# Performance work log

Hardware: AMD Instinct MI355X
Metric: run time of the kernel (lower is better)

## Reference

```python
import jax, jax.numpy as jnp
import numpy as np

B, C, H, W, K = 8, 256, 128, 128, 9
P = K // 2
DN = ('NCHW', 'OIHW', 'NCHW')


def _dw(x, w, pad):
    # depthwise conv: w has shape (C,1,kh,kw), feature_group_count=C
    return jax.lax.conv_general_dilated(
        x, w, window_strides=(1, 1), padding=pad,
        dimension_numbers=DN, feature_group_count=C)


def setup_inputs() -> dict:
    key = jax.random.key(0)
    ks = jax.random.split(key, 6)
    s = 1.0 / np.sqrt(K)
    return {
        'x': jax.random.normal(ks[0], (B, C, H, W), dtype=jnp.float32),
        'wh1': jax.random.normal(ks[1], (C, 1, 1, K), dtype=jnp.float32) * s,
        'wh2': jax.random.normal(ks[2], (C, 1, 1, K), dtype=jnp.float32) * s,
        'wv1': jax.random.normal(ks[3], (C, 1, K, 1), dtype=jnp.float32) * s,
        'wv2': jax.random.normal(ks[4], (C, 1, K, 1), dtype=jnp.float32) * s,
        'wproj': jax.random.normal(ks[5], (C, 4 * C), dtype=jnp.float32) / np.sqrt(4 * C),
    }


def reference(x, wh1, wh2, wv1, wv2, wproj):
    pad_h = ((0, 0), (P, P))  # 1xK conv pads width
    pad_v = ((P, P), (0, 0))  # Kx1 conv pads height
    y = jnp.concatenate([
        _dw(x, wh1, pad_h),
        _dw(x, wh2, pad_h),
        _dw(x, wv1, pad_v),
        _dw(x, wv2, pad_v),
    ], axis=1)  # (B, 4C, H, W)
    out = jnp.einsum('oc,bchw->bohw', wproj, y)  # 1x1 projection
    return jax.nn.relu(out)
```

## Files before the change

### kernel.cpp

```cpp
#include <hip/hip_runtime.h>
#include <hip/hip_bf16.h>

#define BB 8
#define CC 256
#define HH 128
#define WW 128
#define KS 9
#define NPIX (BB*HH*WW)
#define KDIM (4*CC)

typedef __attribute__((ext_vector_type(8))) short bf16x8;
typedef __attribute__((ext_vector_type(4))) float f32x4;

static __device__ __forceinline__ unsigned short f2bf(float f) {
  union { float f; unsigned u; } v; v.f = f;
  unsigned r = v.u + 0x7FFF + ((v.u >> 16) & 1);
  return (unsigned short)(r >> 16);
}
static __device__ __forceinline__ float bf2f(unsigned short u) {
  union { unsigned u; float f; } v; v.u = ((unsigned)u) << 16;
  return v.f;
}

static __device__ __forceinline__ void gload_lds16(const void* g, void* l) {
  __builtin_amdgcn_global_load_lds(
      (const __attribute__((address_space(1))) void*)g,
      (__attribute__((address_space(3))) void*)l, 16, 0, 0);
}

__global__ void prep_kernel(const float* __restrict__ wproj,
                            unsigned short* __restrict__ Ap) {
  int idx = blockIdx.x * 256 + threadIdx.x;
  int o  = idx >> 10;
  int kp = idx & 1023;
  int c  = kp >> 2;
  int t  = kp & 3;
  Ap[idx] = f2bf(wproj[o * 1024 + t * 256 + c]);
}

__global__ void wprep_kernel(const float* __restrict__ wh1,
                             const float* __restrict__ wh2,
                             const float* __restrict__ wv1,
                             const float* __restrict__ wv2,
                             float* __restrict__ wt) {
  int idx = blockIdx.x * 256 + threadIdx.x;
  int c = idx & 255;
  int q = idx >> 8;
  int cv = q / 9, k = q % 9;
  const float* src = (cv == 0) ? wh1 : (cv == 1) ? wh2 : (cv == 2) ? wv1 : wv2;
  wt[idx] = src[c * KS + k];
}

__global__ __launch_bounds__(256)
void transpose_kernel(const float* __restrict__ x,
                      unsigned short* __restrict__ xt) {
  __shared__ float lds[64][65];
  int g   = blockIdx.x;
  int b   = g >> 10;
  int r   = g & 1023;
  int ct  = r >> 8;
  int hwt = r & 255;
  int c0  = ct * 64, hw0 = hwt * 64;
  const float* in = x + (size_t)b * CC * (HH * WW);
  unsigned short* outp = xt + (size_t)b * (HH * WW) * CC;

  int tr  = threadIdx.x >> 4;
  int tc4 = (threadIdx.x & 15) * 4;

#pragma unroll
  for (int s = 0; s < 4; ++s) {
    int row = tr + s * 16;
    float4 v = *(const float4*)(in + (size_t)(c0 + row) * (HH * WW) + hw0 + tc4);
    lds[row][tc4 + 0] = v.x; lds[row][tc4 + 1] = v.y;
    lds[row][tc4 + 2] = v.z; lds[row][tc4 + 3] = v.w;
  }
  __syncthreads();
#pragma unroll
  for (int s = 0; s < 4; ++s) {
    int row_o = tr + s * 16;
    ushort4 o;
    o.x = f2bf(lds[tc4 + 0][row_o]);
    o.y = f2bf(lds[tc4 + 1][row_o]);
    o.z = f2bf(lds[tc4 + 2][row_o]);
    o.w = f2bf(lds[tc4 + 3][row_o]);
    *(ushort4*)(outp + (size_t)(hw0 + row_o) * CC + c0 + tc4) = o;
  }
}

__global__ __launch_bounds__(256)
void conv_kernel(const unsigned short* __restrict__ xt,
                 const float* __restrict__ wt,
                 unsigned short* __restrict__ Y) {
  int g  = blockIdx.x;
  int sb = (g & 7) * 512 + (g >> 3);
  int w  = sb & 127;
  int tq = sb >> 7;
  int hs = tq & 3;
  int b  = tq >> 2;
  int c  = threadIdx.x;

  float W1[KS], W2[KS], W3[KS], W4[KS];
#pragma unroll
  for (int k = 0; k < KS; ++k) {
    W1[k] = wt[(0 * KS + k) * CC + c];
    W2[k] = wt[(1 * KS + k) * CC + c];
    W3[k] = wt[(2 * KS + k) * CC + c];
    W4[k] = wt[(3 * KS + k) * CC + c];
  }

  const unsigned short* xb = xt + (size_t)b * (HH * WW) * CC;
  int h0 = hs * 32;

  float vwin[9];
#pragma unroll
  for (int i = 0; i < 8; ++i) {
    int row = h0 - 4 + i;
    vwin[i] = (row >= 0) ? bf2f(xb[(size_t)(row * WW + w) * CC + c]) : 0.f;
  }

#pragma unroll
  for (int s = 0; s < 32; ++s) {
    int h  = h0 + s;
    int rv = h + 4;
    vwin[8] = (rv < HH) ? bf2f(xb[(size_t)(rv * WW + w) * CC + c]) : 0.f;

    float hwin[9];
#pragma unroll
    for (int j = 0; j < 9; ++j) {
      if (j == 4) { hwin[j] = vwin[4]; continue; }
      int wp = w - 4 + j;
      hwin[j] = (wp >= 0 && wp < WW) ? bf2f(xb[(size_t)(h * WW + wp) * CC + c]) : 0.f;
    }

    float s1 = 0.f, s2 = 0.f, s3 = 0.f, s4 = 0.f;
#pragma unroll
    for (int k = 0; k < KS; ++k) {
      s1 = fmaf(hwin[k], W1[k], s1);
      s2 = fmaf(hwin[k], W2[k], s2);
      s3 = fmaf(vwin[k], W3[k], s3);
      s4 = fmaf(vwin[k], W4[k], s4);
    }
    unsigned u0 = (unsigned)f2bf(s1) | ((unsigned)f2bf(s2) << 16);
    unsigned u1 = (unsigned)f2bf(s3) | ((unsigned)f2bf(s4) << 16);
    size_t p = (size_t)(b * (HH * WW) + h * WW + w);
    *(uint2*)(Y + p * KDIM + c * 4) = make_uint2(u0, u1);

#pragma unroll
    for (int i = 0; i < 8; ++i) vwin[i] = vwin[i + 1];
  }
}

__global__ __launch_bounds__(512)
void gemm_kernel(const unsigned short* __restrict__ Ap,
                 const unsigned short* __restrict__ Yg,
                 float* __restrict__ out) {
  __shared__ short As[256 * 64];
  __shared__ short Bs[128 * 64];

  int bid = blockIdx.x;
  int pt  = (bid & 7) * 128 + (bid >> 3);
  int tid  = threadIdx.x;
  int lane = tid & 63;
  int wv   = tid >> 6;
  int om   = wv & 3;
  int pn   = wv >> 2;
  int l15  = lane & 15;
  int kseg = lane >> 4;

  const short* A  = (const short*)Ap;
  const short* Bg = (const short*)Yg + (size_t)pt * 128 * KDIM;

  int srow = tid >> 3;
  int skc  = (tid & 7) * 8;

  f32x4 acc[4][4] = {};

  for (int k0 = 0; k0 < KDIM; k0 += 64) {
#pragma unroll
    for (int i = 0; i < 4; ++i) {
      int rr = i * 64 + srow;
      gload_lds16(A + (size_t)rr * KDIM + k0 + skc, &As[rr * 64 + skc]);
    }
#pragma unroll
    for (int i = 0; i < 2; ++i) {
      int rr = i * 64 + srow;
      gload_lds16(Bg + (size_t)rr * KDIM + k0 + skc, &Bs[rr * 64 + skc]);
    }
    __syncthreads();
#pragma unroll
    for (int kk = 0; kk < 2; ++kk) {
      bf16x8 af[4], bfr[4];
#pragma unroll
      for (int m = 0; m < 4; ++m)
        af[m] = *(const bf16x8*)&As[(om * 64 + m * 16 + l15) * 64 + kk * 32 + kseg * 8];
#pragma unroll
      for (int n = 0; n < 4; ++n)
        bfr[n] = *(const bf16x8*)&Bs[(pn * 64 + n * 16 + l15) * 64 + kk * 32 + kseg * 8];
#pragma unroll
      for (int m = 0; m < 4; ++m)
#pragma unroll
        for (int n = 0; n < 4; ++n)
          acc[m][n] = __builtin_amdgcn_mfma_f32_16x16x32_bf16(af[m], bfr[n],
                                                              acc[m][n], 0, 0, 0);
    }
    __syncthreads();
  }

  int b = pt >> 7, h = pt & 127;
#pragma unroll
  for (int m = 0; m < 4; ++m) {
#pragma unroll
    for (int n = 0; n < 4; ++n) {
#pragma unroll
      for (int r = 0; r < 4; ++r) {
        int o = om * 64 + m * 16 + kseg * 4 + r;
        int w = pn * 64 + n * 16 + l15;
        out[((size_t)(b * 256 + o) << 14) + (h << 7) + w] =
            fmaxf(acc[m][n][r], 0.f);
      }
    }
  }
}

extern "C" void kernel_launch(void* const* d_in, const int* in_sizes, int n_in,
                              void* d_out, int out_size, void* d_ws, size_t ws_size,
                              hipStream_t stream) {
  (void)in_sizes; (void)n_in; (void)out_size; (void)ws_size;
  const float* x     = (const float*)d_in[0];
  const float* wh1   = (const float*)d_in[1];
  const float* wh2   = (const float*)d_in[2];
  const float* wv1   = (const float*)d_in[3];
  const float* wv2   = (const float*)d_in[4];
  const float* wproj = (const float*)d_in[5];
  float* out = (float*)d_out;

  char* wsb = (char*)d_ws;
  unsigned short* Yg = (unsigned short*)wsb;
  unsigned short* Xt = (unsigned short*)(wsb + (size_t)NPIX * KDIM * 2);
  unsigned short* Ap = (unsigned short*)(wsb + (size_t)NPIX * KDIM * 2
                                             + (size_t)NPIX * CC * 2);
  float* Wt = (float*)(wsb + (size_t)NPIX * KDIM * 2
                           + (size_t)NPIX * CC * 2 + (size_t)CC * KDIM * 2);

  hipLaunchKernelGGL(prep_kernel, dim3(1024), dim3(256), 0, stream, wproj, Ap);
  hipLaunchKernelGGL(wprep_kernel, dim3(36), dim3(256), 0, stream,
                     wh1, wh2, wv1, wv2, Wt);
  hipLaunchKernelGGL(transpose_kernel, dim3(8192), dim3(256), 0, stream, x, Xt);
  hipLaunchKernelGGL(conv_kernel, dim3(4096), dim3(256), 0, stream, Xt, Wt, Yg);
  hipLaunchKernelGGL(gemm_kernel, dim3(1024), dim3(512), 0, stream, Ap, Yg, out);
}
```

Before: 605.6 us.

## Slide conv window along width and stage GEMM epilogue through LDS for vector stores

The conv kernel now gives each block one row and a 32-column strip, sliding the horizontal window along width and loading the vertical taps fresh for each pixel. Before, each block walked down 32 rows of one column. This changes the locality of the transposed input and makes consecutive Y writes contiguous per block. The GEMM epilogue now writes accumulators to LDS in 32-row chunks and reads them back so each thread issues two float4 stores per output row. This replaces the scattered scalar stores. The cost is eight extra LDS round trips with barriers, and more global loads per pixel in the conv, relying on the cache to absorb them.

```diff
diff --git a/kernel.cpp b/kernel.cpp
--- a/kernel.cpp
+++ b/kernel.cpp
@@ -91,13 +91,12 @@
 void conv_kernel(const unsigned short* __restrict__ xt,
                  const float* __restrict__ wt,
                  unsigned short* __restrict__ Y) {
-  int g  = blockIdx.x;
-  int sb = (g & 7) * 512 + (g >> 3);
-  int w  = sb & 127;
-  int tq = sb >> 7;
-  int hs = tq & 3;
-  int b  = tq >> 2;
-  int c  = threadIdx.x;
+  int g    = blockIdx.x;
+  int b    = g & 7;
+  int rest = g >> 3;
+  int h    = rest >> 2;
+  int ws   = rest & 3;
+  int c    = threadIdx.x;
 
   float W1[KS], W2[KS], W3[KS], W4[KS];
 #pragma unroll
@@ -109,27 +108,26 @@
   }
 
   const unsigned short* xb = xt + (size_t)b * (HH * WW) * CC;
-  int h0 = hs * 32;
-
-  float vwin[9];
-#pragma unroll
-  for (int i = 0; i < 8; ++i) {
-    int row = h0 - 4 + i;
-    vwin[i] = (row >= 0) ? bf2f(xb[(size_t)(row * WW + w) * CC + c]) : 0.f;
-  }
-
-#pragma unroll
+  int w0 = ws * 32;
+
+  float hwin[9];
+#pragma unroll
+  for (int i = 0; i < 9; ++i) {
+    int wp = w0 - 4 + i;
+    hwin[i] = (wp >= 0 && wp < WW) ? bf2f(xb[((size_t)h * WW + wp) * CC + c]) : 0.f;
+  }
+
+  unsigned short* ybase = Y + ((size_t)((b * HH + h) * WW)) * KDIM + c * 4;
+
+#pragma unroll 4
   for (int s = 0; s < 32; ++s) {
-    int h  = h0 + s;
-    int rv = h + 4;
-    vwin[8] = (rv < HH) ? bf2f(xb[(size_t)(rv * WW + w) * CC + c]) : 0.f;
-
-    float hwin[9];
-#pragma unroll
-    for (int j = 0; j < 9; ++j) {
-      if (j == 4) { hwin[j] = vwin[4]; continue; }
-      int wp = w - 4 + j;
-      hwin[j] = (wp >= 0 && wp < WW) ? bf2f(xb[(size_t)(h * WW + wp) * CC + c]) : 0.f;
+    int w = w0 + s;
+    float vv[9];
+#pragma unroll
+    for (int k = 0; k < 9; ++k) {
+      if (k == 4) { vv[k] = hwin[4]; continue; }
+      int r = h - 4 + k;
+      vv[k] = (r >= 0 && r < HH) ? bf2f(xb[((size_t)r * WW + w) * CC + c]) : 0.f;
     }
 
     float s1 = 0.f, s2 = 0.f, s3 = 0.f, s4 = 0.f;
@@ -137,16 +135,17 @@
     for (int k = 0; k < KS; ++k) {
       s1 = fmaf(hwin[k], W1[k], s1);
       s2 = fmaf(hwin[k], W2[k], s2);
-      s3 = fmaf(vwin[k], W3[k], s3);
-      s4 = fmaf(vwin[k], W4[k], s4);
+      s3 = fmaf(vv[k],   W3[k], s3);
+      s4 = fmaf(vv[k],   W4[k], s4);
     }
     unsigned u0 = (unsigned)f2bf(s1) | ((unsigned)f2bf(s2) << 16);
     unsigned u1 = (unsigned)f2bf(s3) | ((unsigned)f2bf(s4) << 16);
-    size_t p = (size_t)(b * (HH * WW) + h * WW + w);
-    *(uint2*)(Y + p * KDIM + c * 4) = make_uint2(u0, u1);
-
-#pragma unroll
-    for (int i = 0; i < 8; ++i) vwin[i] = vwin[i + 1];
+    *(uint2*)(ybase + (size_t)w * KDIM) = make_uint2(u0, u1);
+
+#pragma unroll
+    for (int i = 0; i < 8; ++i) hwin[i] = hwin[i + 1];
+    int wn = w + 5;
+    hwin[8] = (wn < WW) ? bf2f(xb[((size_t)h * WW + wn) * CC + c]) : 0.f;
   }
 }
 
@@ -206,19 +205,39 @@
     __syncthreads();
   }
 
-  int b = pt >> 7, h = pt & 127;
-#pragma unroll
-  for (int m = 0; m < 4; ++m) {
-#pragma unroll
-    for (int n = 0; n < 4; ++n) {
-#pragma unroll
-      for (int r = 0; r < 4; ++r) {
-        int o = om * 64 + m * 16 + kseg * 4 + r;
-        int w = pn * 64 + n * 16 + l15;
-        out[((size_t)(b * 256 + o) << 14) + (h << 7) + w] =
-            fmaxf(acc[m][n][r], 0.f);
+  float* Ls = (float*)As;
+  const int LP = 132;
+  int b2 = pt >> 7, h2 = pt & 127;
+  int er = tid >> 4;
+  int ec = (tid & 15) * 8;
+  size_t obase = ((size_t)(b2 * 256) << 14) + (h2 << 7);
+
+#pragma unroll
+  for (int oc = 0; oc < 8; ++oc) {
+    __syncthreads();
+    if (om == (oc >> 1)) {
+      int mb = (oc & 1) * 2;
+#pragma unroll
+      for (int mm = 0; mm < 2; ++mm) {
+#pragma unroll
+        for (int n = 0; n < 4; ++n) {
+#pragma unroll
+          for (int r = 0; r < 4; ++r) {
+            int row = mm * 16 + kseg * 4 + r;
+            int col = pn * 64 + n * 16 + l15;
+            Ls[row * LP + col] = acc[mb + mm][n][r];
+          }
+        }
       }
     }
+    __syncthreads();
+    float4 v0 = *(const float4*)&Ls[er * LP + ec];
+    float4 v1 = *(const float4*)&Ls[er * LP + ec + 4];
+    size_t oaddr = obase + ((size_t)(oc * 32 + er) << 14) + ec;
+    *(float4*)&out[oaddr] = make_float4(fmaxf(v0.x, 0.f), fmaxf(v0.y, 0.f),
+                                        fmaxf(v0.z, 0.f), fmaxf(v0.w, 0.f));
+    *(float4*)&out[oaddr + 4] = make_float4(fmaxf(v1.x, 0.f), fmaxf(v1.y, 0.f),
+                                            fmaxf(v1.z, 0.f), fmaxf(v1.w, 0.f));
   }
 }
 
```

Result: faster. 590.7 us (-2.5%).
